# Optimization experiments

Hardware: AMD Instinct MI355X
Metric: run time of the kernel (lower is better)

Reference implementation:

```python
import jax, jax.numpy as jnp
import numpy as np

N_HEADS = 16


def setup_inputs() -> dict:
    key = jax.random.key(0)
    ks = jax.random.split(key, 9)
    B, S, D = 2, 2048, 1024
    sc = 0.02
    return {
        'x': jax.random.normal(ks[0], (B, S, D), jnp.float32),
        'Wq': jax.random.normal(ks[1], (D, D), jnp.float32) * sc,
        'bq': jax.random.normal(ks[2], (D,), jnp.float32) * sc,
        'Wk': jax.random.normal(ks[3], (D, D), jnp.float32) * sc,
        'bk': jax.random.normal(ks[4], (D,), jnp.float32) * sc,
        'Wv': jax.random.normal(ks[5], (D, D), jnp.float32) * sc,
        'bv': jax.random.normal(ks[6], (D,), jnp.float32) * sc,
        'Wo': jax.random.normal(ks[7], (D, D), jnp.float32) * sc,
        'bo': jax.random.normal(ks[8], (D,), jnp.float32) * sc,
    }


def reference(x, Wq, bq, Wk, bk, Wv, bv, Wo, bo):
    # Chunked causal prefill. The chunk-wise mask (q_pos >= kv_pos over the
    # growing KV cache) is mathematically identical to full causal attention,
    # so we compute it as one vectorized masked softmax attention.
    B, S, D = x.shape
    H = N_HEADS
    hd = D // H

    def proj(W, b):
        # torch Linear: y = x @ W.T + b ; then split heads -> [B,H,S,hd]
        y = jnp.einsum('bsd,ed->bse', x, W) + b
        return y.reshape(B, S, H, hd).transpose(0, 2, 1, 3)

    q = proj(Wq, bq)
    k = proj(Wk, bk)
    v = proj(Wv, bv)

    scores = jnp.einsum('bhqd,bhkd->bhqk', q, k) / jnp.sqrt(jnp.asarray(hd, x.dtype))
    causal = jnp.tril(jnp.ones((S, S), dtype=bool))  # [S,S]
    scores = jnp.where(causal[None, None], scores, jnp.asarray(-jnp.inf, scores.dtype))
    attn = jax.nn.softmax(scores, axis=-1)
    ctx = jnp.einsum('bhqk,bhkd->bhqd', attn, v)  # [B,H,S,hd]
    ctx = ctx.transpose(0, 2, 1, 3).reshape(B, S, D)
    out = jnp.einsum('bsd,ed->bse', ctx, Wo) + bo
    return out
```

## Files before the change

kernel.cpp:

```cpp
#include <hip/hip_runtime.h>
#include <cstdint>
#include <math.h>

typedef _Float16 f16;
typedef _Float16 f16x2 __attribute__((ext_vector_type(2)));
typedef _Float16 f16x4 __attribute__((ext_vector_type(4)));
typedef _Float16 f16x8 __attribute__((ext_vector_type(8)));
typedef __fp16   h16x2 __attribute__((ext_vector_type(2)));
typedef float    f32x4 __attribute__((ext_vector_type(4)));

__device__ __forceinline__ f32x4 mfma16(f16x8 a, f16x8 b, f32x4 c) {
  return __builtin_amdgcn_mfma_f32_16x16x32_f16(a, b, c, 0, 0, 0);
}
__device__ __forceinline__ void gl2lds16(const f16* g, f16* l) {
  __builtin_amdgcn_global_load_lds((__attribute__((address_space(1))) void*)(g),
                                   (__attribute__((address_space(3))) void*)(l),
                                   16, 0, 0);
}
__device__ __forceinline__ float fexp2(float x) { return __builtin_amdgcn_exp2f(x); }
__device__ __forceinline__ f16x2 pkrtz(float a, float b) {
  h16x2 r = __builtin_amdgcn_cvt_pkrtz(a, b);
  return __builtin_bit_cast(f16x2, r);
}
__device__ __forceinline__ float dot2acc(f16x2 a, f16x2 b, float c) {
#if __has_builtin(__builtin_amdgcn_fdot2)
  return __builtin_amdgcn_fdot2(__builtin_bit_cast(h16x2, a),
                                __builtin_bit_cast(h16x2, b), c, false);
#else
  return c + (float)a[0] * (float)b[0] + (float)a[1] * (float)b[1];
#endif
}

__global__ __launch_bounds__(256) void cvt_kernel(
    const float* __restrict__ x,  const float* __restrict__ wq, const float* __restrict__ wk,
    const float* __restrict__ wv, const float* __restrict__ wo,
    f16* __restrict__ xh, f16* __restrict__ wqkvh, f16* __restrict__ woh)
{
  const int seg = blockIdx.y;
  const float* src; f16* dst; int n;
  if      (seg == 0) { src = x;  dst = xh;              n = 4194304; }
  else if (seg == 1) { src = wq; dst = wqkvh;           n = 1048576; }
  else if (seg == 2) { src = wk; dst = wqkvh + 1048576; n = 1048576; }
  else if (seg == 3) { src = wv; dst = wqkvh + 2097152; n = 1048576; }
  else               { src = wo; dst = woh;             n = 1048576; }
  const int idx = (int)(blockIdx.x * 256 + threadIdx.x) * 8;
  if (idx >= n) return;
  f32x4 a = *(const f32x4*)(src + idx);
  f32x4 b = *(const f32x4*)(src + idx + 4);
  f16x8 h;
  h[0] = (f16)a[0]; h[1] = (f16)a[1]; h[2] = (f16)a[2]; h[3] = (f16)a[3];
  h[4] = (f16)b[0]; h[5] = (f16)b[1]; h[6] = (f16)b[2]; h[7] = (f16)b[3];
  *(f16x8*)(dst + idx) = h;
}

__global__ __launch_bounds__(256) void gemm_qkv(
    const f16* __restrict__ A, const f16* __restrict__ B,
    const float* __restrict__ bias0, const float* __restrict__ bias1, const float* __restrict__ bias2,
    f16* __restrict__ Qp, f16* __restrict__ Kp, f16* __restrict__ Vp)
{
  constexpr int K = 1024;
  __shared__ __align__(16) f16 As[128 * 32];
  __shared__ __align__(16) f16 Bs[128 * 32];
  const int tid  = threadIdx.x;
  const int wave = tid >> 6, lane = tid & 63;
  const int quad = lane >> 4, col = lane & 15;
  const int tile_m = blockIdx.y * 128, tile_n = blockIdx.x * 128;
  const int mb = (wave >> 1) * 64, nb = (wave & 1) * 64;
  const int srow = lane >> 2, scol = (lane & 3) * 8;
  const f16* gA = A + (size_t)(tile_m + wave * 32 + srow) * K + scol;
  const f16* gB = B + (size_t)(tile_n + wave * 32 + srow) * K + scol;
  f16* lA = As + wave * 1024;
  f16* lB = Bs + wave * 1024;

  f32x4 acc[4][4] = {};
  for (int k0 = 0; k0 < K; k0 += 32) {
    gl2lds16(gA + k0,          lA);
    gl2lds16(gA + 16 * K + k0, lA + 512);
    gl2lds16(gB + k0,          lB);
    gl2lds16(gB + 16 * K + k0, lB + 512);
    __syncthreads();
    f16x8 af[4], bf[4];
    #pragma unroll
    for (int i = 0; i < 4; ++i)
      af[i] = *(const f16x8*)&As[(mb + i * 16 + col) * 32 + quad * 8];
    #pragma unroll
    for (int j = 0; j < 4; ++j)
      bf[j] = *(const f16x8*)&Bs[(nb + j * 16 + col) * 32 + quad * 8];
    #pragma unroll
    for (int i = 0; i < 4; ++i)
      #pragma unroll
      for (int j = 0; j < 4; ++j)
        acc[i][j] = mfma16(af[i], bf[j], acc[i][j]);
    __syncthreads();
  }

  #pragma unroll
  for (int j = 0; j < 4; ++j) {
    const int gn = tile_n + nb + j * 16 + col;
    const int which = gn >> 10;
    const int d = gn & 1023;
    const float* bp = (which == 0) ? bias0 : (which == 1) ? bias1 : bias2;
    f16* dst        = (which == 0) ? Qp    : (which == 1) ? Kp    : Vp;
    const float bvv = bp[d];
    const float qs  = (which == 0) ? 0.18033688f : 1.0f;
    const int h = d >> 6, hi = d & 63;
    #pragma unroll
    for (int i = 0; i < 4; ++i) {
      #pragma unroll
      for (int r = 0; r < 4; ++r) {
        const int gm = tile_m + mb + i * 16 + quad * 4 + r;
        const int bb = gm >> 11, s = gm & 2047;
        dst[(((size_t)bb * 16 + h) * 2048 + s) * 64 + hi] = (f16)((acc[i][j][r] + bvv) * qs);
      }
    }
  }
}

__global__ __launch_bounds__(256) void vtrans_kernel(
    const f16* __restrict__ Vh, f16* __restrict__ Vt)
{
  __shared__ __align__(16) f16 t[64][72];
  const int bh = blockIdx.y;
  const int s0 = blockIdx.x * 64;
  const int tid = threadIdx.x;
  const int sr = tid >> 2, dc = (tid & 3) * 16;
  const size_t ib = ((size_t)bh * 2048 + s0 + sr) * 64 + dc;
  f16x8 v0 = *(const f16x8*)&Vh[ib];
  f16x8 v1 = *(const f16x8*)&Vh[ib + 8];
  *(f16x8*)&t[sr][dc]     = v0;
  *(f16x8*)&t[sr][dc + 8] = v1;
  __syncthreads();
  const int d = tid >> 2, sc = (tid & 3) * 16;
  f16x8 o0, o1;
  #pragma unroll
  for (int j = 0; j < 8; ++j) { o0[j] = t[sc + j][d]; o1[j] = t[sc + 8 + j][d]; }
  const size_t ob = ((size_t)bh * 64 + d) * 2048 + s0 + sc;
  *(f16x8*)&Vt[ob]     = o0;
  *(f16x8*)&Vt[ob + 8] = o1;
}

__global__ __launch_bounds__(256, 4) void attn_kernel(
    const f16* __restrict__ Q, const f16* __restrict__ K, const f16* __restrict__ Vt,
    f16* __restrict__ ctx)
{
  __shared__ __align__(16) f16 Ks[2][64 * 72];
  __shared__ __align__(16) f16 Vts[2][64 * 72];
  __shared__ __align__(16) f16 Ps[4][2][16 * 72];

  const int bh  = blockIdx.x;
  const int yy  = blockIdx.y;
  const int p   = (yy < 8) ? yy : 23 - yy;
  const int qlong = 31 - p, qshort = p;
  const int tid = threadIdx.x;
  const int wave = tid >> 6, lane = tid & 63;
  const int quad = lane >> 4, col = lane & 15;
  const int b = bh >> 4, h = bh & 15;
  const size_t base = (size_t)bh * 2048 * 64;
  const size_t vtb  = (size_t)bh * 64 * 2048;

  int srow[2], sc8[2];
  #pragma unroll
  for (int i = 0; i < 2; ++i) {
    const int flat = tid + i * 256;
    srow[i] = flat >> 3;
    sc8[i]  = (flat & 7) * 8;
  }

  const int qa = qlong * 64 + wave * 16;
  const int qb = qshort * 64 + wave * 16;
  const f16x8 bqa0 = *(const f16x8*)&Q[base + (size_t)(qa + col) * 64 + quad * 8];
  const f16x8 bqa1 = *(const f16x8*)&Q[base + (size_t)(qa + col) * 64 + 32 + quad * 8];
  const f16x8 bqb0 = *(const f16x8*)&Q[base + (size_t)(qb + col) * 64 + quad * 8];
  const f16x8 bqb1 = *(const f16x8*)&Q[base + (size_t)(qb + col) * 64 + 32 + quad * 8];

  f32x4 cta[4] = {}, ctb[4] = {};
  float la = 0.f, lb2 = 0.f;

  f16x8 kr[2], vr[2];
  auto gload = [&](int t) {
    #pragma unroll
    for (int i = 0; i < 2; ++i) {
      kr[i] = *(const f16x8*)&K[base + (size_t)(t * 64 + srow[i]) * 64 + sc8[i]];
      vr[i] = *(const f16x8*)&Vt[vtb + (size_t)srow[i] * 2048 + t * 64 + sc8[i]];
    }
  };
  auto swrite = [&](int buf) {
    #pragma unroll
    for (int i = 0; i < 2; ++i) {
      *(f16x8*)&Ks[buf][srow[i] * 72 + sc8[i]]  = kr[i];
      *(f16x8*)&Vts[buf][srow[i] * 72 + sc8[i]] = vr[i];
    }
  };

  const int nIter = qlong + 1;

  gload(0);
  __syncthreads();
  swrite(0);
  gload(1);

  for (int t = 0; t < nIter; ++t) {
    const int cur = t & 1;
    __syncthreads();
    if (t + 1 < nIter) {
      swrite(cur ^ 1);
      if (t + 2 < nIter) gload(t + 2);
    }
    const bool doB = (t <= qshort);

    f32x4 sa[4], sb[4];
    #pragma unroll
    for (int jt = 0; jt < 4; ++jt) {
      const int kro = (jt * 16 + col) * 72;
      const f16x8 ak0 = *(const f16x8*)&Ks[cur][kro + quad * 8];
      const f16x8 ak1 = *(const f16x8*)&Ks[cur][kro + 32 + quad * 8];
      f32x4 za = {};
      za = mfma16(ak0, bqa0, za);
      sa[jt] = mfma16(ak1, bqa1, za);
      if (doB) {
        f32x4 zb = {};
        zb = mfma16(ak0, bqb0, zb);
        sb[jt] = mfma16(ak1, bqb1, zb);
      }
    }

    if (t == qlong) {
      #pragma unroll
      for (int jt = 0; jt < 4; ++jt) {
        const int kg = t * 64 + jt * 16 + quad * 4;
        #pragma unroll
        for (int r = 0; r < 4; ++r)
          if (kg + r > qa + col) sa[jt][r] = -1e30f;
      }
    }
    if (t == qshort) {
      #pragma unroll
      for (int jt = 0; jt < 4; ++jt) {
        const int kg = t * 64 + jt * 16 + quad * 4;
        #pragma unroll
        for (int r = 0; r < 4; ++r)
          if (kg + r > qb + col) sb[jt][r] = -1e30f;
      }
    }

    const f16x2 one2 = {(_Float16)1.f, (_Float16)1.f};

    {
      float rs = 0.f;
      #pragma unroll
      for (int jt = 0; jt < 4; ++jt) {
        const f16x2 a01 = pkrtz(fexp2(sa[jt][0]), fexp2(sa[jt][1]));
        const f16x2 a23 = pkrtz(fexp2(sa[jt][2]), fexp2(sa[jt][3]));
        rs = dot2acc(a01, one2, rs);
        rs = dot2acc(a23, one2, rs);
        f16x4 pw; pw[0] = a01[0]; pw[1] = a01[1]; pw[2] = a23[0]; pw[3] = a23[1];
        *(f16x4*)&Ps[wave][0][col * 72 + jt * 16 + quad * 4] = pw;
      }
      la += rs;
    }

    if (doB) {
      float rs = 0.f;
      #pragma unroll
      for (int jt = 0; jt < 4; ++jt) {
        const f16x2 a01 = pkrtz(fexp2(sb[jt][0]), fexp2(sb[jt][1]));
        const f16x2 a23 = pkrtz(fexp2(sb[jt][2]), fexp2(sb[jt][3]));
        rs = dot2acc(a01, one2, rs);
        rs = dot2acc(a23, one2, rs);
        f16x4 pw; pw[0] = a01[0]; pw[1] = a01[1]; pw[2] = a23[0]; pw[3] = a23[1];
        *(f16x4*)&Ps[wave][1][col * 72 + jt * 16 + quad * 4] = pw;
      }
      lb2 += rs;
    }

    __asm__ volatile("s_waitcnt lgkmcnt(0)" ::: "memory");

    const f16x8 apa0 = *(const f16x8*)&Ps[wave][0][col * 72 + quad * 8];
    const f16x8 apa1 = *(const f16x8*)&Ps[wave][0][col * 72 + 32 + quad * 8];
    if (doB) {
      const f16x8 apb0 = *(const f16x8*)&Ps[wave][1][col * 72 + quad * 8];
      const f16x8 apb1 = *(const f16x8*)&Ps[wave][1][col * 72 + 32 + quad * 8];
      #pragma unroll
      for (int jd = 0; jd < 4; ++jd) {
        const int vro = (jd * 16 + col) * 72;
        const f16x8 bv0 = *(const f16x8*)&Vts[cur][vro + quad * 8];
        const f16x8 bv1 = *(const f16x8*)&Vts[cur][vro + 32 + quad * 8];
        cta[jd] = mfma16(apa1, bv1, mfma16(apa0, bv0, cta[jd]));
        ctb[jd] = mfma16(apb1, bv1, mfma16(apb0, bv0, ctb[jd]));
      }
    } else {
      #pragma unroll
      for (int jd = 0; jd < 4; ++jd) {
        const int vro = (jd * 16 + col) * 72;
        const f16x8 bv0 = *(const f16x8*)&Vts[cur][vro + quad * 8];
        const f16x8 bv1 = *(const f16x8*)&Vts[cur][vro + 32 + quad * 8];
        cta[jd] = mfma16(apa1, bv1, mfma16(apa0, bv0, cta[jd]));
      }
    }
  }

  {
    la += __shfl_xor(la, 16);
    la += __shfl_xor(la, 32);
    f32x4 lva;
    #pragma unroll
    for (int r = 0; r < 4; ++r) lva[r] = __shfl(la, quad * 4 + r);
    #pragma unroll
    for (int jd = 0; jd < 4; ++jd) {
      #pragma unroll
      for (int r = 0; r < 4; ++r) {
        const int qga = qa + quad * 4 + r;
        const int d = h * 64 + jd * 16 + col;
        ctx[((size_t)b * 2048 + qga) * 1024 + d] = (f16)(cta[jd][r] / lva[r]);
      }
    }
  }
  {
    lb2 += __shfl_xor(lb2, 16);
    lb2 += __shfl_xor(lb2, 32);
    f32x4 lvb;
    #pragma unroll
    for (int r = 0; r < 4; ++r) lvb[r] = __shfl(lb2, quad * 4 + r);
    #pragma unroll
    for (int jd = 0; jd < 4; ++jd) {
      #pragma unroll
      for (int r = 0; r < 4; ++r) {
        const int qgb = qb + quad * 4 + r;
        const int d = h * 64 + jd * 16 + col;
        ctx[((size_t)b * 2048 + qgb) * 1024 + d] = (f16)(ctb[jd][r] / lvb[r]);
      }
    }
  }
}

__global__ __launch_bounds__(256) void gemm_o(
    const f16* __restrict__ A, const f16* __restrict__ B, const float* __restrict__ bias,
    float* __restrict__ Out)
{
  constexpr int K = 1024;
  __shared__ __align__(16) f16 As[128 * 32];
  __shared__ __align__(16) f16 Bs[64 * 32];
  const int tid  = threadIdx.x;
  const int wave = tid >> 6, lane = tid & 63;
  const int quad = lane >> 4, col = lane & 15;
  const int tile_m = blockIdx.y * 128, tile_n = blockIdx.x * 64;
  const int mb = wave * 32;
  const int srow = lane >> 2, scol = (lane & 3) * 8;
  const f16* gA = A + (size_t)(tile_m + wave * 32 + srow) * K + scol;
  const f16* gB = B + (size_t)(tile_n + wave * 16 + srow) * K + scol;
  f16* lA = As + wave * 1024;
  f16* lB = Bs + wave * 512;

  f32x4 acc[2][4] = {};
  for (int k0 = 0; k0 < K; k0 += 32) {
    gl2lds16(gA + k0,          lA);
    gl2lds16(gA + 16 * K + k0, lA + 512);
    gl2lds16(gB + k0,          lB);
    __syncthreads();
    f16x8 af[2], bf[4];
    #pragma unroll
    for (int i = 0; i < 2; ++i)
      af[i] = *(const f16x8*)&As[(mb + i * 16 + col) * 32 + quad * 8];
    #pragma unroll
    for (int j = 0; j < 4; ++j)
      bf[j] = *(const f16x8*)&Bs[(j * 16 + col) * 32 + quad * 8];
    #pragma unroll
    for (int i = 0; i < 2; ++i)
      #pragma unroll
      for (int j = 0; j < 4; ++j)
        acc[i][j] = mfma16(af[i], bf[j], acc[i][j]);
    __syncthreads();
  }

  #pragma unroll
  for (int j = 0; j < 4; ++j) {
    const int gn = tile_n + j * 16 + col;
    const float bvv = bias[gn];
    #pragma unroll
    for (int i = 0; i < 2; ++i) {
      #pragma unroll
      for (int r = 0; r < 4; ++r) {
        const int gm = tile_m + mb + i * 16 + quad * 4 + r;
        Out[(size_t)gm * 1024 + gn] = acc[i][j][r] + bvv;
      }
    }
  }
}

extern "C" void kernel_launch(void* const* d_in, const int* in_sizes, int n_in,
                              void* d_out, int out_size, void* d_ws, size_t ws_size,
                              hipStream_t stream)
{
  const float* x  = (const float*)d_in[0];
  const float* Wq = (const float*)d_in[1];
  const float* bq = (const float*)d_in[2];
  const float* Wk = (const float*)d_in[3];
  const float* bk = (const float*)d_in[4];
  const float* Wv = (const float*)d_in[5];
  const float* bv = (const float*)d_in[6];
  const float* Wo = (const float*)d_in[7];
  const float* bo = (const float*)d_in[8];
  float* out = (float*)d_out;

  f16* ws = (f16*)d_ws;
  const size_t M1 = 1048576;
  f16* xh    = ws;
  f16* wqkvh = ws + 4  * M1;
  f16* woh   = ws + 7  * M1;
  f16* Qh    = ws + 8  * M1;
  f16* Kh    = ws + 12 * M1;
  f16* Vh    = ws + 16 * M1;
  f16* Vth   = ws + 20 * M1;
  f16* ctxh  = ws + 24 * M1;

  cvt_kernel<<<dim3(2048, 5), 256, 0, stream>>>(x, Wq, Wk, Wv, Wo, xh, wqkvh, woh);
  gemm_qkv<<<dim3(24, 32), 256, 0, stream>>>(xh, wqkvh, bq, bk, bv, Qh, Kh, Vh);
  vtrans_kernel<<<dim3(32, 32), 256, 0, stream>>>(Vh, Vth);
  attn_kernel<<<dim3(32, 16), 256, 0, stream>>>(Qh, Kh, Vth, ctxh);
  gemm_o<<<dim3(16, 32), 256, 0, stream>>>(ctxh, woh, bo, out);
}
```

Baseline: 186.6 us.

## Double-buffer LDS in projection GEMMs and compact conversion kernel grid

Both projection GEMMs now use two LDS buffers. The next K-slice's global-to-LDS load is issued right after the barrier, so it overlaps the MFMA work on the current slice, and one barrier per iteration goes away. The conversion kernel switches from a 2D grid, where most weight-segment blocks exited early, to a flat 1D grid with only useful blocks. This doubles LDS use per block, which may lower occupancy. The correctness of the single-barrier scheme depends on how the asynchronous LDS loads are waited on before the barrier.

```diff
diff --git a/kernel.cpp b/kernel.cpp
--- a/kernel.cpp
+++ b/kernel.cpp
@@ -36,15 +36,18 @@
     const float* __restrict__ wv, const float* __restrict__ wo,
     f16* __restrict__ xh, f16* __restrict__ wqkvh, f16* __restrict__ woh)
 {
-  const int seg = blockIdx.y;
-  const float* src; f16* dst; int n;
-  if      (seg == 0) { src = x;  dst = xh;              n = 4194304; }
-  else if (seg == 1) { src = wq; dst = wqkvh;           n = 1048576; }
-  else if (seg == 2) { src = wk; dst = wqkvh + 1048576; n = 1048576; }
-  else if (seg == 3) { src = wv; dst = wqkvh + 2097152; n = 1048576; }
-  else               { src = wo; dst = woh;             n = 1048576; }
-  const int idx = (int)(blockIdx.x * 256 + threadIdx.x) * 8;
-  if (idx >= n) return;
+  const int blk = blockIdx.x;
+  const float* src; f16* dst; int off;
+  if (blk < 2048)      { src = x;  dst = xh;              off = blk; }
+  else {
+    const int wseg = (blk - 2048) >> 9;
+    off = (blk - 2048) & 511;
+    if      (wseg == 0) { src = wq; dst = wqkvh; }
+    else if (wseg == 1) { src = wk; dst = wqkvh + 1048576; }
+    else if (wseg == 2) { src = wv; dst = wqkvh + 2097152; }
+    else                { src = wo; dst = woh; }
+  }
+  const int idx = off * 2048 + (int)threadIdx.x * 8;
   f32x4 a = *(const f32x4*)(src + idx);
   f32x4 b = *(const f32x4*)(src + idx + 4);
   f16x8 h;
@@ -59,8 +62,8 @@
     f16* __restrict__ Qp, f16* __restrict__ Kp, f16* __restrict__ Vp)
 {
   constexpr int K = 1024;
-  __shared__ __align__(16) f16 As[128 * 32];
-  __shared__ __align__(16) f16 Bs[128 * 32];
+  __shared__ __align__(16) f16 As[2][128 * 32];
+  __shared__ __align__(16) f16 Bs[2][128 * 32];
   const int tid  = threadIdx.x;
   const int wave = tid >> 6, lane = tid & 63;
   const int quad = lane >> 4, col = lane & 15;
@@ -69,29 +72,32 @@
   const int srow = lane >> 2, scol = (lane & 3) * 8;
   const f16* gA = A + (size_t)(tile_m + wave * 32 + srow) * K + scol;
   const f16* gB = B + (size_t)(tile_n + wave * 32 + srow) * K + scol;
-  f16* lA = As + wave * 1024;
-  f16* lB = Bs + wave * 1024;
+
+  auto stage = [&](int buf, int k0) {
+    gl2lds16(gA + k0,          &As[buf][wave * 1024]);
+    gl2lds16(gA + 16 * K + k0, &As[buf][wave * 1024 + 512]);
+    gl2lds16(gB + k0,          &Bs[buf][wave * 1024]);
+    gl2lds16(gB + 16 * K + k0, &Bs[buf][wave * 1024 + 512]);
+  };
 
   f32x4 acc[4][4] = {};
+  stage(0, 0);
   for (int k0 = 0; k0 < K; k0 += 32) {
-    gl2lds16(gA + k0,          lA);
-    gl2lds16(gA + 16 * K + k0, lA + 512);
-    gl2lds16(gB + k0,          lB);
-    gl2lds16(gB + 16 * K + k0, lB + 512);
+    const int cur = (k0 >> 5) & 1;
     __syncthreads();
+    if (k0 + 32 < K) stage(cur ^ 1, k0 + 32);
     f16x8 af[4], bf[4];
     #pragma unroll
     for (int i = 0; i < 4; ++i)
-      af[i] = *(const f16x8*)&As[(mb + i * 16 + col) * 32 + quad * 8];
+      af[i] = *(const f16x8*)&As[cur][(mb + i * 16 + col) * 32 + quad * 8];
     #pragma unroll
     for (int j = 0; j < 4; ++j)
-      bf[j] = *(const f16x8*)&Bs[(nb + j * 16 + col) * 32 + quad * 8];
+      bf[j] = *(const f16x8*)&Bs[cur][(nb + j * 16 + col) * 32 + quad * 8];
     #pragma unroll
     for (int i = 0; i < 4; ++i)
       #pragma unroll
       for (int j = 0; j < 4; ++j)
         acc[i][j] = mfma16(af[i], bf[j], acc[i][j]);
-    __syncthreads();
   }
 
   #pragma unroll
@@ -338,8 +344,8 @@
     float* __restrict__ Out)
 {
   constexpr int K = 1024;
-  __shared__ __align__(16) f16 As[128 * 32];
-  __shared__ __align__(16) f16 Bs[64 * 32];
+  __shared__ __align__(16) f16 As[2][128 * 32];
+  __shared__ __align__(16) f16 Bs[2][64 * 32];
   const int tid  = threadIdx.x;
   const int wave = tid >> 6, lane = tid & 63;
   const int quad = lane >> 4, col = lane & 15;
@@ -348,28 +354,31 @@
   const int srow = lane >> 2, scol = (lane & 3) * 8;
   const f16* gA = A + (size_t)(tile_m + wave * 32 + srow) * K + scol;
   const f16* gB = B + (size_t)(tile_n + wave * 16 + srow) * K + scol;
-  f16* lA = As + wave * 1024;
-  f16* lB = Bs + wave * 512;
+
+  auto stage = [&](int buf, int k0) {
+    gl2lds16(gA + k0,          &As[buf][wave * 1024]);
+    gl2lds16(gA + 16 * K + k0, &As[buf][wave * 1024 + 512]);
+    gl2lds16(gB + k0,          &Bs[buf][wave * 512]);
+  };
 
   f32x4 acc[2][4] = {};
+  stage(0, 0);
   for (int k0 = 0; k0 < K; k0 += 32) {
-    gl2lds16(gA + k0,          lA);
-    gl2lds16(gA + 16 * K + k0, lA + 512);
-    gl2lds16(gB + k0,          lB);
+    const int cur = (k0 >> 5) & 1;
     __syncthreads();
+    if (k0 + 32 < K) stage(cur ^ 1, k0 + 32);
     f16x8 af[2], bf[4];
     #pragma unroll
     for (int i = 0; i < 2; ++i)
-      af[i] = *(const f16x8*)&As[(mb + i * 16 + col) * 32 + quad * 8];
+      af[i] = *(const f16x8*)&As[cur][(mb + i * 16 + col) * 32 + quad * 8];
     #pragma unroll
     for (int j = 0; j < 4; ++j)
-      bf[j] = *(const f16x8*)&Bs[(j * 16 + col) * 32 + quad * 8];
+      bf[j] = *(const f16x8*)&Bs[cur][(j * 16 + col) * 32 + quad * 8];
     #pragma unroll
     for (int i = 0; i < 2; ++i)
       #pragma unroll
       for (int j = 0; j < 4; ++j)
         acc[i][j] = mfma16(af[i], bf[j], acc[i][j]);
-    __syncthreads();
   }
 
   #pragma unroll
@@ -413,7 +422,7 @@
   f16* Vth   = ws + 20 * M1;
   f16* ctxh  = ws + 24 * M1;
 
-  cvt_kernel<<<dim3(2048, 5), 256, 0, stream>>>(x, Wq, Wk, Wv, Wo, xh, wqkvh, woh);
+  cvt_kernel<<<4096, 256, 0, stream>>>(x, Wq, Wk, Wv, Wo, xh, wqkvh, woh);
   gemm_qkv<<<dim3(24, 32), 256, 0, stream>>>(xh, wqkvh, bq, bk, bv, Qh, Kh, Vh);
   vtrans_kernel<<<dim3(32, 32), 256, 0, stream>>>(Vh, Vth);
   attn_kernel<<<dim3(32, 16), 256, 0, stream>>>(Qh, Kh, Vth, ctxh);
```

Result: no change. 189.9 us (+1.7%).
